# Performance work log

Measured on AMD Instinct MI355X. Metric: run time of the kernel, lower is better.

## Reference

```python
import jax, jax.numpy as jnp
import numpy as np

N = 131072        # total nodes
E = 786432        # total edges (avg degree 6)
NSEG = 128        # number of (graph, config) segments
SEG = N // NSEG   # nodes per segment (equal-size ragged layout)
G = 8             # graphs in batch
S = NSEG // G     # segments (configs) per graph
NF, NCF, OP_DIM = 112, 14, 64
FD = NF + NCF + OP_DIM        # 190 = node_feature_dim
GIN, HID, NOPS = 256, 512, 120


def _linear_init(key, fan_in, fan_out):
    lim = 1.0 / np.sqrt(fan_in)
    return jax.random.uniform(key, (fan_in, fan_out), jnp.float32, -lim, lim)


def setup_inputs() -> dict:
    key = jax.random.key(0)
    ks = jax.random.split(key, 24)
    inp = {
        "node_features": jax.random.normal(ks[0], (N, NF), jnp.float32),
        "node_config_features": jax.random.normal(ks[1], (N, NCF), jnp.float32),
        "node_ops": jax.random.randint(ks[2], (N,), 0, NOPS),
        "edges": jax.random.randint(ks[3], (2, E), 0, N),
        # cumulative exclusive end index of each segment
        "node_separation": (jnp.arange(1, NSEG + 1) * SEG).astype(jnp.int32),
        # which graph each segment belongs to (sorted, S segments per graph)
        "batches": jnp.repeat(jnp.arange(G), S).astype(jnp.int32),
        # parameters
        "emb": jax.random.normal(ks[4], (NOPS, OP_DIM), jnp.float32),
        "W1": _linear_init(ks[5], FD, FD * 2), "b1": jnp.zeros((FD * 2,), jnp.float32),
        "W2": _linear_init(ks[6], FD * 2, GIN), "b2": jnp.zeros((GIN,), jnp.float32),
        "Wl1": _linear_init(ks[7], GIN, HID), "bl1": jnp.zeros((HID,), jnp.float32),
        "Wr1": _linear_init(ks[8], GIN, HID),
        "Wl2": _linear_init(ks[9], HID, HID), "bl2": jnp.zeros((HID,), jnp.float32),
        "Wr2": _linear_init(ks[10], HID, HID),
        "Wl3": _linear_init(ks[11], HID, HID), "bl3": jnp.zeros((HID,), jnp.float32),
        "Wr3": _linear_init(ks[12], HID, HID),
        "Wf": _linear_init(ks[13], HID, 1), "bf": jnp.zeros((1,), jnp.float32),
    }
    return inp


def _l2norm(x, eps=1e-12):
    # F.normalize(p=2): x / max(||x||, eps)
    return x / jnp.maximum(jnp.linalg.norm(x, axis=-1, keepdims=True), eps)


def _sage_conv(x, src, dst, Wl, bl, Wr):
    # mean aggregation of source features onto destination nodes
    msum = jax.ops.segment_sum(x[src], dst, num_segments=N)
    cnt = jax.ops.segment_sum(jnp.ones((src.shape[0],), x.dtype), dst, num_segments=N)
    mean = msum / jnp.maximum(cnt, 1.0)[:, None]
    out = mean @ Wl + bl + x @ Wr   # lin_l(aggr) + lin_r(x), bias only on lin_l
    return _l2norm(out)             # graphsage_normalize=True


def reference(node_features, node_config_features, node_ops, edges, node_separation,
              batches, emb, W1, b1, W2, b2, Wl1, bl1, Wr1, Wl2, bl2, Wr2,
              Wl3, bl3, Wr3, Wf, bf):
    # embedding + feature concat (dropouts are identity at eval)
    op_e = emb[node_ops]                                       # [N, 64]
    x = jnp.concatenate([node_features, node_config_features, op_e], axis=1)  # [N, 190]
    # node feature MLP with L2 normalization over feature dim
    h = jax.nn.relu(x @ W1 + b1)
    h = _l2norm(h @ W2 + b2)                                   # [N, 256]
    # 3-layer GraphSAGE (ReLU between layers, none after last)
    src, dst = edges[0], edges[1]
    h = jax.nn.relu(_sage_conv(h, src, dst, Wl1, bl1, Wr1))
    h = jax.nn.relu(_sage_conv(h, src, dst, Wl2, bl2, Wr2))
    h = _sage_conv(h, src, dst, Wl3, bl3, Wr3)                 # [N, 512]
    # ragged segment-sum: node i belongs to first segment with end index > i
    seg_ids = jnp.searchsorted(node_separation, jnp.arange(N), side="right")
    seg = jax.ops.segment_sum(h, seg_ids, num_segments=NSEG)   # [128, 512]
    # group segments by graph (batches is sorted with S segments per graph)
    within = jnp.arange(NSEG) % S
    agg = jnp.zeros((G, S, HID), h.dtype).at[batches, within].set(seg)
    # final classifier: Linear(512 -> 1), squeeze
    out = (agg @ Wf + bf)[..., 0]                              # [G, S]
    return out
```

## Files before the change

kernel.cpp:

```cpp
#include <hip/hip_runtime.h>
#include <hip/hip_bf16.h>
#include <stdint.h>

#define NN   131072
#define EE   786432
#define NSEGC 128
#define SSC  16
#define NFD  112
#define NCFD 14
#define OPD  64
#define FDIM 190
#define FD2  380
#define GIN  256
#define HID  512

typedef unsigned short u16;
typedef unsigned int   u32;
typedef __attribute__((ext_vector_type(8))) short bf16x8;
typedef __attribute__((ext_vector_type(4))) float f32x4;

__device__ __forceinline__ float b2f(u16 v) { u32 u = ((u32)v) << 16; return __builtin_bit_cast(float, u); }
__device__ __forceinline__ u16 f2b(float f) {
  u32 u = __builtin_bit_cast(u32, f);
  u32 r = (u + 0x7fffu + ((u >> 16) & 1u)) >> 16;
  return (u16)r;
}
__device__ __forceinline__ void unpk8(uint4 q, float* f) {
  f[0] = __builtin_bit_cast(float, q.x << 16);
  f[1] = __builtin_bit_cast(float, q.x & 0xffff0000u);
  f[2] = __builtin_bit_cast(float, q.y << 16);
  f[3] = __builtin_bit_cast(float, q.y & 0xffff0000u);
  f[4] = __builtin_bit_cast(float, q.z << 16);
  f[5] = __builtin_bit_cast(float, q.z & 0xffff0000u);
  f[6] = __builtin_bit_cast(float, q.w << 16);
  f[7] = __builtin_bit_cast(float, q.w & 0xffff0000u);
}
__device__ __forceinline__ void gload16(const void* g, void* lds) {
  __builtin_amdgcn_global_load_lds((const __attribute__((address_space(1))) void*)g,
                                   (__attribute__((address_space(3))) void*)lds, 16, 0, 0);
}

__global__ void k_diag(float* out, float v) { out[threadIdx.x] = v; }

__global__ void k_count(const int* __restrict__ dst, int* __restrict__ deg) {
  int e = blockIdx.x * 256 + threadIdx.x;
  if (e < EE) atomicAdd(&deg[dst[e]], 1);
}

__global__ __launch_bounds__(1024) void k_bsum(const int* __restrict__ deg, int* __restrict__ bsum) {
  __shared__ int ws[16];
  int tid = threadIdx.x;
  int lane = tid & 63, w = tid >> 6;
  int x = deg[blockIdx.x * 1024 + tid];
  #pragma unroll
  for (int off = 32; off; off >>= 1) x += __shfl_xor(x, off, 64);
  if (lane == 0) ws[w] = x;
  __syncthreads();
  if (tid == 0) {
    int t = 0;
    #pragma unroll
    for (int i = 0; i < 16; ++i) t += ws[i];
    bsum[blockIdx.x] = t;
  }
}

__global__ void k_bscan(const int* __restrict__ bsum, int* __restrict__ boff) {
  __shared__ int w0sum;
  int t = threadIdx.x;
  int lane = t & 63;
  int orig = bsum[t];
  int x = orig;
  #pragma unroll
  for (int off = 1; off < 64; off <<= 1) {
    int v = __shfl_up(x, off, 64);
    if (lane >= off) x += v;
  }
  if (t == 63) w0sum = x;
  __syncthreads();
  int excl = x - orig;
  if (t >= 64) excl += w0sum;
  boff[t] = excl;
}

__global__ __launch_bounds__(1024) void k_iptr(const int* __restrict__ deg, const int* __restrict__ boff,
                                               int* __restrict__ indptr) {
  __shared__ int wsum[16];
  int b = blockIdx.x, tid = threadIdx.x;
  int lane = tid & 63, w = tid >> 6;
  int x = deg[b * 1024 + tid];
  #pragma unroll
  for (int off = 1; off < 64; off <<= 1) {
    int v = __shfl_up(x, off, 64);
    if (lane >= off) x += v;
  }
  if (lane == 63) wsum[w] = x;
  __syncthreads();
  int woff = 0;
  #pragma unroll
  for (int i = 0; i < 16; ++i) if (i < w) woff += wsum[i];
  indptr[b * 1024 + tid + 1] = boff[b] + woff + x;
  if (b == 0 && tid == 0) indptr[0] = 0;
}

__global__ void k_fill(const int* __restrict__ src, const int* __restrict__ dst,
                       const int* __restrict__ indptr, int* __restrict__ cur,
                       int* __restrict__ colidx) {
  int e = blockIdx.x * 256 + threadIdx.x;
  if (e < EE) {
    int d = dst[e];
    int p = atomicAdd(&cur[d], 1);
    colidx[indptr[d] + p] = src[e];
  }
}

__global__ void k_wcvt(const float* __restrict__ Wl, const float* __restrict__ Wr,
                       const int kin, u16* __restrict__ WbT) {
  int keff = kin * 2;
  int idx = blockIdx.x * 256 + threadIdx.x;
  int k4 = idx % (keff >> 2);
  int n  = idx / (keff >> 2);
  if (n >= HID) return;
  int k0 = k4 << 2;
  u16 o[4];
  #pragma unroll
  for (int j = 0; j < 4; ++j) {
    int k = k0 + j;
    float v = (k < kin) ? Wl[(size_t)k * HID + n] : Wr[(size_t)(k - kin) * HID + n];
    o[j] = f2b(v);
  }
  uint2 pk;
  pk.x = (u32)o[0] | ((u32)o[1] << 16);
  pk.y = (u32)o[2] | ((u32)o[3] << 16);
  *(uint2*)(WbT + (size_t)n * keff + k0) = pk;
}

__global__ void k_w1cvt(const float* __restrict__ W1, u16* __restrict__ W1p) {
  int t = blockIdx.x / 6, s = blockIdx.x % 6;
  int lane = threadIdx.x;
  int lg = lane >> 4, lc = lane & 15;
  int n = t * 16 + lc;
  bf16x8 v;
  #pragma unroll
  for (int j = 0; j < 8; ++j) {
    int k = s * 32 + lg * 8 + j;
    float f = (k < FDIM && n < FD2) ? W1[(size_t)k * FD2 + n] : 0.f;
    v[j] = (short)f2b(f);
  }
  *(bf16x8*)(W1p + ((size_t)blockIdx.x * 64 + lane) * 8) = v;
}

__global__ void k_w2cvt(const float* __restrict__ W2, u16* __restrict__ W2p) {
  int t = blockIdx.x / 12, s = blockIdx.x % 12;
  int lane = threadIdx.x;
  int lg = lane >> 4, lc = lane & 15;
  int n = t * 16 + lc;
  bf16x8 v;
  #pragma unroll
  for (int j = 0; j < 8; ++j) {
    int k = s * 32 + lg * 8 + j;
    float f = (k < FD2) ? W2[(size_t)k * GIN + n] : 0.f;
    v[j] = (short)f2b(f);
  }
  *(bf16x8*)(W2p + ((size_t)blockIdx.x * 64 + lane) * 8) = v;
}

__global__ __launch_bounds__(512, 4) void k_mlpm(const float* __restrict__ nf, const float* __restrict__ ncf,
                                                 const int* __restrict__ ops, const float* __restrict__ emb,
                                                 const u16* __restrict__ W1p, const float* __restrict__ b1,
                                                 const u16* __restrict__ W2p, const float* __restrict__ b2,
                                                 u16* __restrict__ hA) {
  __shared__ u16 Xs[64 * 200];
  __shared__ u16 H1s[64 * 392];
  const int m0 = blockIdx.x * 64;
  const int tid = threadIdx.x;
  const int lane = tid & 63;
  const int wid = tid >> 6;
  const int lg = lane >> 4;
  const int lc = lane & 15;

  for (int idx = tid; idx < 64 * NFD; idx += 512) {
    int r = idx / NFD, k = idx - r * NFD;
    Xs[r * 200 + k] = f2b(nf[(size_t)(m0 + r) * NFD + k]);
  }
  for (int idx = tid; idx < 64 * NCFD; idx += 512) {
    int r = idx / NCFD, k = idx - r * NCFD;
    Xs[r * 200 + NFD + k] = f2b(ncf[(size_t)(m0 + r) * NCFD + k]);
  }
  for (int idx = tid; idx < 64 * OPD; idx += 512) {
    int r = idx >> 6, k = idx & 63;
    Xs[r * 200 + NFD + NCFD + k] = f2b(emb[(size_t)ops[m0 + r] * OPD + k]);
  }
  if (tid < 128) {
    int r = tid >> 1;
    Xs[r * 200 + FDIM + (tid & 1)] = 0;
  }
  __syncthreads();

  f32x4 acc1[4][3];
  #pragma unroll
  for (int mt = 0; mt < 4; ++mt)
    #pragma unroll
    for (int nt = 0; nt < 3; ++nt) acc1[mt][nt] = (f32x4){0.f, 0.f, 0.f, 0.f};
  #pragma unroll
  for (int s = 0; s < 6; ++s) {
    bf16x8 af[4];
    #pragma unroll
    for (int mt = 0; mt < 4; ++mt)
      af[mt] = *(const bf16x8*)(Xs + (mt * 16 + lc) * 200 + s * 32 + lg * 8);
    #pragma unroll
    for (int nt = 0; nt < 3; ++nt) {
      int t = wid * 3 + nt;
      bf16x8 bfr = *(const bf16x8*)(W1p + ((size_t)(t * 6 + s) * 64 + lane) * 8);
      #pragma unroll
      for (int mt = 0; mt < 4; ++mt)
        acc1[mt][nt] = __builtin_amdgcn_mfma_f32_16x16x32_bf16(af[mt], bfr, acc1[mt][nt], 0, 0, 0);
    }
  }
  #pragma unroll
  for (int nt = 0; nt < 3; ++nt) {
    int n = (wid * 3 + nt) * 16 + lc;
    float bias = b1[n < FD2 ? n : FD2 - 1];
    #pragma unroll
    for (int mt = 0; mt < 4; ++mt)
      #pragma unroll
      for (int r = 0; r < 4; ++r) {
        float v = acc1[mt][nt][r] + bias;
        H1s[(mt * 16 + lg * 4 + r) * 392 + n] = f2b(v > 0.f ? v : 0.f);
      }
  }
  __syncthreads();

  f32x4 acc2[4][2];
  #pragma unroll
  for (int mt = 0; mt < 4; ++mt)
    #pragma unroll
    for (int nt = 0; nt < 2; ++nt) acc2[mt][nt] = (f32x4){0.f, 0.f, 0.f, 0.f};
  #pragma unroll
  for (int s = 0; s < 12; ++s) {
    bf16x8 af[4];
    #pragma unroll
    for (int mt = 0; mt < 4; ++mt)
      af[mt] = *(const bf16x8*)(H1s + (mt * 16 + lc) * 392 + s * 32 + lg * 8);
    #pragma unroll
    for (int nt = 0; nt < 2; ++nt) {
      int t = wid * 2 + nt;
      bf16x8 bfr = *(const bf16x8*)(W2p + ((size_t)(t * 12 + s) * 64 + lane) * 8);
      #pragma unroll
      for (int mt = 0; mt < 4; ++mt)
        acc2[mt][nt] = __builtin_amdgcn_mfma_f32_16x16x32_bf16(af[mt], bfr, acc2[mt][nt], 0, 0, 0);
    }
  }
  float* ssq = (float*)Xs;
  float bias2[2];
  #pragma unroll
  for (int nt = 0; nt < 2; ++nt) bias2[nt] = b2[(wid * 2 + nt) * 16 + lc];
  #pragma unroll
  for (int mt = 0; mt < 4; ++mt)
    #pragma unroll
    for (int r = 0; r < 4; ++r) {
      float s = 0.f;
      #pragma unroll
      for (int nt = 0; nt < 2; ++nt) {
        float v = acc2[mt][nt][r] + bias2[nt];
        acc2[mt][nt][r] = v;
        s += v * v;
      }
      s += __shfl_xor(s, 1, 64);
      s += __shfl_xor(s, 2, 64);
      s += __shfl_xor(s, 4, 64);
      s += __shfl_xor(s, 8, 64);
      if (lc == 0) ssq[(mt * 16 + lg * 4 + r) * 8 + wid] = s;
    }
  __syncthreads();
  float scl[4][4];
  #pragma unroll
  for (int mt = 0; mt < 4; ++mt)
    #pragma unroll
    for (int r = 0; r < 4; ++r) {
      const float* p = ssq + (mt * 16 + lg * 4 + r) * 8;
      float t = ((p[0] + p[1]) + (p[2] + p[3])) + ((p[4] + p[5]) + (p[6] + p[7]));
      scl[mt][r] = 1.f / fmaxf(sqrtf(t), 1e-12f);
    }
  u16* T = H1s;
  #pragma unroll
  for (int mt = 0; mt < 4; ++mt)
    #pragma unroll
    for (int nt = 0; nt < 2; ++nt)
      #pragma unroll
      for (int r = 0; r < 4; ++r)
        T[(mt * 16 + lg * 4 + r) * 264 + (wid * 2 + nt) * 16 + lc] =
            f2b(acc2[mt][nt][r] * scl[mt][r]);
  __syncthreads();
  #pragma unroll
  for (int it = 0; it < 4; ++it) {
    int flat = it * 512 + tid;
    int row = flat >> 5, ch = flat & 31;
    uint4 v = *(const uint4*)(T + row * 264 + ch * 8);
    *(uint4*)(hA + (size_t)(m0 + row) * HID + ch * 8) = v;
  }
}

template<int F>
__global__ __launch_bounds__(256) void k_agg(const u16* __restrict__ h, int8_t* __restrict__ M8,
                                             float* __restrict__ Msc,
                                             const int* __restrict__ indptr, const int* __restrict__ colidx) {
  int d = blockIdx.x * 4 + (threadIdx.x >> 6);
  int lane = threadIdx.x & 63;
  float acc[F];
  #pragma unroll
  for (int i = 0; i < F; ++i) acc[i] = 0.f;
  int s0 = indptr[d], s1 = indptr[d + 1];
  int e = s0;
  for (; e + 3 < s1; e += 4) {
    int sa = colidx[e], sb = colidx[e + 1], sc = colidx[e + 2], sd = colidx[e + 3];
    if constexpr (F == 8) {
      uint4 qa = *(const uint4*)(h + (size_t)sa * HID + lane * 8);
      uint4 qb = *(const uint4*)(h + (size_t)sb * HID + lane * 8);
      uint4 qc = *(const uint4*)(h + (size_t)sc * HID + lane * 8);
      uint4 qd = *(const uint4*)(h + (size_t)sd * HID + lane * 8);
      float fa[8], fb[8], fc[8], fd[8];
      unpk8(qa, fa); unpk8(qb, fb); unpk8(qc, fc); unpk8(qd, fd);
      #pragma unroll
      for (int i = 0; i < 8; ++i) acc[i] += (fa[i] + fb[i]) + (fc[i] + fd[i]);
    } else {
      uint2 qa = *(const uint2*)(h + (size_t)sa * HID + lane * 4);
      uint2 qb = *(const uint2*)(h + (size_t)sb * HID + lane * 4);
      uint2 qc = *(const uint2*)(h + (size_t)sc * HID + lane * 4);
      uint2 qd = *(const uint2*)(h + (size_t)sd * HID + lane * 4);
      acc[0] += (__builtin_bit_cast(float, qa.x << 16) + __builtin_bit_cast(float, qb.x << 16))
              + (__builtin_bit_cast(float, qc.x << 16) + __builtin_bit_cast(float, qd.x << 16));
      acc[1] += (__builtin_bit_cast(float, qa.x & 0xffff0000u) + __builtin_bit_cast(float, qb.x & 0xffff0000u))
              + (__builtin_bit_cast(float, qc.x & 0xffff0000u) + __builtin_bit_cast(float, qd.x & 0xffff0000u));
      acc[2] += (__builtin_bit_cast(float, qa.y << 16) + __builtin_bit_cast(float, qb.y << 16))
              + (__builtin_bit_cast(float, qc.y << 16) + __builtin_bit_cast(float, qd.y << 16));
      acc[3] += (__builtin_bit_cast(float, qa.y & 0xffff0000u) + __builtin_bit_cast(float, qb.y & 0xffff0000u))
              + (__builtin_bit_cast(float, qc.y & 0xffff0000u) + __builtin_bit_cast(float, qd.y & 0xffff0000u));
    }
  }
  for (; e < s1; ++e) {
    int s = colidx[e];
    const u16* p = h + (size_t)s * HID + lane * F;
    if constexpr (F == 8) {
      uint4 q = *(const uint4*)p;
      float f[8]; unpk8(q, f);
      #pragma unroll
      for (int i = 0; i < 8; ++i) acc[i] += f[i];
    } else {
      uint2 q = *(const uint2*)p;
      acc[0] += __builtin_bit_cast(float, q.x << 16);
      acc[1] += __builtin_bit_cast(float, q.x & 0xffff0000u);
      acc[2] += __builtin_bit_cast(float, q.y << 16);
      acc[3] += __builtin_bit_cast(float, q.y & 0xffff0000u);
    }
  }
  int dgi = s1 - s0;
  float inv = 1.f / (float)(dgi > 1 ? dgi : 1);
  float m = 0.f;
  #pragma unroll
  for (int i = 0; i < F; ++i) { acc[i] *= inv; m = fmaxf(m, fabsf(acc[i])); }
  #pragma unroll
  for (int off = 32; off; off >>= 1) m = fmaxf(m, __shfl_xor(m, off, 64));
  float scale = (m > 0.f) ? (m / 127.f) : 1.f;
  float rscl = 1.f / scale;
  int q[F];
  #pragma unroll
  for (int i = 0; i < F; ++i) {
    int t = (int)__builtin_rintf(acc[i] * rscl);
    q[i] = t < -127 ? -127 : (t > 127 ? 127 : t);
  }
  int8_t* row = M8 + (size_t)d * HID;
  if constexpr (F == 8) {
    uint2 o;
    o.x = (u32)(q[0] & 255) | ((u32)(q[1] & 255) << 8) | ((u32)(q[2] & 255) << 16) | ((u32)(q[3] & 255) << 24);
    o.y = (u32)(q[4] & 255) | ((u32)(q[5] & 255) << 8) | ((u32)(q[6] & 255) << 16) | ((u32)(q[7] & 255) << 24);
    *(uint2*)(row + lane * 8) = o;
  } else {
    u32 o = (u32)(q[0] & 255) | ((u32)(q[1] & 255) << 8) | ((u32)(q[2] & 255) << 16) | ((u32)(q[3] & 255) << 24);
    *(u32*)(row + lane * 4) = o;
  }
  if (lane == 0) Msc[d] = scale;
}

template<int KIN, bool RELU, bool FUSE>
__global__ __launch_bounds__(512, 4) void k_sagem(const u16* __restrict__ hA,
                                                  const int8_t* __restrict__ M8,
                                                  const float* __restrict__ Msc,
                                                  const u16* __restrict__ WbT,
                                                  const float* __restrict__ bl,
                                                  u16* __restrict__ outp,
                                                  const float* __restrict__ Wf,
                                                  float* __restrict__ partial) {
  constexpr int KEFF = 2 * KIN;
  constexpr int KSTEPS = KEFF / 64;
  __shared__ unsigned char smem[73728];
  u16* As = (u16*)smem;
  u16* Bs = (u16*)(smem + 8192);
  const int m0 = blockIdx.x * 64;
  const int tid = threadIdx.x;
  const int lane = tid & 63;
  const int wid = tid >> 6;
  const int lg = lane >> 4;
  const int lc = lane & 15;

  f32x4 acc[4][4];
  #pragma unroll
  for (int mt = 0; mt < 4; ++mt)
    #pragma unroll
    for (int nt = 0; nt < 4; ++nt) acc[mt][nt] = (f32x4){0.f, 0.f, 0.f, 0.f};

  for (int t = 0; t < KSTEPS; ++t) {
    const int kt = t * 64;
    __syncthreads();
    if (kt < KIN) {
      int r = tid >> 3, c = tid & 7;
      int row = m0 + r;
      float sc = Msc[row];
      uint2 q = *(const uint2*)(M8 + (size_t)row * HID + kt + c * 8);
      float f[8];
      #pragma unroll
      for (int i = 0; i < 4; ++i) f[i]     = (float)((int)(q.x << (24 - 8 * i)) >> 24) * sc;
      #pragma unroll
      for (int i = 0; i < 4; ++i) f[4 + i] = (float)((int)(q.y << (24 - 8 * i)) >> 24) * sc;
      bf16x8 v;
      #pragma unroll
      for (int i = 0; i < 8; ++i) v[i] = (short)f2b(f[i]);
      *(bf16x8*)(As + r * 64 + ((c ^ (r & 7)) << 3)) = v;
    } else {
      int r = wid * 8 + (lane >> 3);
      int c = (lane & 7) ^ (lane >> 3);
      gload16(hA + (size_t)(m0 + r) * HID + (kt - KIN) + c * 8, As + wid * 512);
    }
    #pragma unroll
    for (int i = 0; i < 8; ++i) {
      int R = wid * 64 + i * 8;
      int n = R + (lane >> 3);
      int c = (lane & 7) ^ (lane >> 3);
      gload16(WbT + (size_t)n * KEFF + kt + c * 8, Bs + R * 64);
    }
    __syncthreads();
    __builtin_amdgcn_s_setprio(1);
    #pragma unroll
    for (int s = 0; s < 2; ++s) {
      bf16x8 af[4];
      #pragma unroll
      for (int mt = 0; mt < 4; ++mt) {
        int r = mt * 16 + lc;
        int c = (s * 4 + lg) ^ (r & 7);
        af[mt] = *(const bf16x8*)(As + r * 64 + (c << 3));
      }
      #pragma unroll
      for (int nt = 0; nt < 4; ++nt) {
        int n = wid * 64 + nt * 16 + lc;
        int c = (s * 4 + lg) ^ (n & 7);
        bf16x8 bfr = *(const bf16x8*)(Bs + n * 64 + (c << 3));
        #pragma unroll
        for (int mt = 0; mt < 4; ++mt)
          acc[mt][nt] = __builtin_amdgcn_mfma_f32_16x16x32_bf16(af[mt], bfr, acc[mt][nt], 0, 0, 0);
      }
    }
    __builtin_amdgcn_s_setprio(0);
  }
  __syncthreads();

  float* ssq = (float*)(smem + 66560);
  float bias[4];
  #pragma unroll
  for (int nt = 0; nt < 4; ++nt) bias[nt] = bl[wid * 64 + nt * 16 + lc];
  #pragma unroll
  for (int mt = 0; mt < 4; ++mt) {
    #pragma unroll
    for (int r = 0; r < 4; ++r) {
      float s = 0.f;
      #pragma unroll
      for (int nt = 0; nt < 4; ++nt) {
        float v = acc[mt][nt][r] + bias[nt];
        acc[mt][nt][r] = v;
        s += v * v;
      }
      s += __shfl_xor(s, 1, 64);
      s += __shfl_xor(s, 2, 64);
      s += __shfl_xor(s, 4, 64);
      s += __shfl_xor(s, 8, 64);
      if (lc == 0) ssq[(mt * 16 + lg * 4 + r) * 8 + wid] = s;
    }
  }
  __syncthreads();
  float scl[4][4];
  #pragma unroll
  for (int mt = 0; mt < 4; ++mt)
    #pragma unroll
    for (int r = 0; r < 4; ++r) {
      const float* p = ssq + (mt * 16 + lg * 4 + r) * 8;
      float t = ((p[0] + p[1]) + (p[2] + p[3])) + ((p[4] + p[5]) + (p[6] + p[7]));
      scl[mt][r] = 1.f / fmaxf(sqrtf(t), 1e-12f);
    }
  if constexpr (FUSE) {
    float wf[4];
    #pragma unroll
    for (int nt = 0; nt < 4; ++nt) wf[nt] = Wf[wid * 64 + nt * 16 + lc];
    float s = 0.f;
    #pragma unroll
    for (int mt = 0; mt < 4; ++mt)
      #pragma unroll
      for (int r = 0; r < 4; ++r) {
        float rs = scl[mt][r];
        #pragma unroll
        for (int nt = 0; nt < 4; ++nt) s += acc[mt][nt][r] * rs * wf[nt];
      }
    #pragma unroll
    for (int off = 32; off; off >>= 1) s += __shfl_xor(s, off, 64);
    float* red = (float*)(smem + 68608);
    if (lane == 0) red[wid] = s;
    __syncthreads();
    if (tid == 0) {
      float t = 0.f;
      #pragma unroll
      for (int i = 0; i < 8; ++i) t += red[i];
      partial[blockIdx.x] = t;
    }
  } else {
    u16* T = (u16*)smem;
    #pragma unroll
    for (int mt = 0; mt < 4; ++mt)
      #pragma unroll
      for (int r = 0; r < 4; ++r) {
        int trow = mt * 16 + lg * 4 + r;
        #pragma unroll
        for (int nt = 0; nt < 4; ++nt) {
          float v = acc[mt][nt][r] * scl[mt][r];
          if (RELU) v = v > 0.f ? v : 0.f;
          T[trow * 520 + wid * 64 + nt * 16 + lc] = f2b(v);
        }
      }
    __syncthreads();
    #pragma unroll
    for (int it = 0; it < 8; ++it) {
      int flat = it * 512 + tid;
      int row = flat >> 6, ch = flat & 63;
      uint4 v = *(const uint4*)(T + row * 520 + ch * 8);
      *(uint4*)(outp + (size_t)(m0 + row) * HID + ch * 8) = v;
    }
  }
}

__global__ void k_fred(const float* __restrict__ partial, const float* __restrict__ bfp,
                       const int* __restrict__ batches, float* __restrict__ outp) {
  int s = threadIdx.x;
  float t = bfp[0];
  #pragma unroll
  for (int i = 0; i < 16; ++i) t += partial[s * 16 + i];
  outp[batches[s] * SSC + (s & (SSC - 1))] = t;
}

extern "C" void kernel_launch(void* const* d_in, const int* in_sizes, int n_in,
                              void* d_out, int out_size, void* d_ws, size_t ws_size,
                              hipStream_t stream) {
  const float* nf   = (const float*)d_in[0];
  const float* ncf  = (const float*)d_in[1];
  const int*   ops  = (const int*)d_in[2];
  const int*   edges = (const int*)d_in[3];
  const int*   sep  = (const int*)d_in[4];
  const int*   batches = (const int*)d_in[5];
  const float* emb  = (const float*)d_in[6];
  const float* W1   = (const float*)d_in[7];  const float* b1 = (const float*)d_in[8];
  const float* W2   = (const float*)d_in[9];  const float* b2 = (const float*)d_in[10];
  const float* Wl1  = (const float*)d_in[11]; const float* bl1 = (const float*)d_in[12]; const float* Wr1 = (const float*)d_in[13];
  const float* Wl2  = (const float*)d_in[14]; const float* bl2 = (const float*)d_in[15]; const float* Wr2 = (const float*)d_in[16];
  const float* Wl3  = (const float*)d_in[17]; const float* bl3 = (const float*)d_in[18]; const float* Wr3 = (const float*)d_in[19];
  const float* Wf   = (const float*)d_in[20]; const float* bfp = (const float*)d_in[21];
  float* outp = (float*)d_out;

  const size_t OFF_M8  = (size_t)NN * HID * 2;
  const size_t OFF_MSC = OFF_M8 + (size_t)NN * HID;
  const size_t OFF_IP  = OFF_MSC + (size_t)NN * 4;
  const size_t OFF_CI  = OFF_IP + (((size_t)(NN + 1) * 4 + 255) & ~(size_t)255);
  const size_t OFF_W1  = OFF_CI + (size_t)EE * 4;
  const size_t OFF_W2  = OFF_W1 + (size_t)HID * 512 * 2;
  const size_t OFF_W3  = OFF_W2 + (size_t)HID * 1024 * 2;
  const size_t NEED    = OFF_W3 + (size_t)HID * 1024 * 2;
  if (ws_size < NEED) {
    k_diag<<<1, 128, 0, stream>>>(outp, (float)((double)ws_size / 1048576.0));
    return;
  }

  char* ws = (char*)d_ws;
  u16*    hA     = (u16*)ws;
  int8_t* M8     = (int8_t*)(ws + OFF_M8);
  float*  Msc    = (float*)(ws + OFF_MSC);
  int*    indptr = (int*)(ws + OFF_IP);
  int*    colidx = (int*)(ws + OFF_CI);
  u16*    Wb1    = (u16*)(ws + OFF_W1);
  u16*    Wb2    = (u16*)(ws + OFF_W2);
  u16*    Wb3    = (u16*)(ws + OFF_W3);
  int*    deg    = (int*)hA;
  int*    cur    = (int*)(ws + (size_t)NN * 4);
  int*    bsum   = (int*)(ws + (size_t)NN * 8);
  int*    boff   = (int*)(ws + (size_t)NN * 8 + 512);
  u16*    W1p    = (u16*)M8;
  u16*    W2p    = (u16*)(ws + OFF_M8 + 262144);
  float*  partials = (float*)Wb1;

  const int* esrc = edges;
  const int* edst = edges + EE;

  hipMemsetAsync(deg, 0, (size_t)NN * 4, stream);
  k_count<<<EE / 256, 256, 0, stream>>>(edst, deg);
  k_bsum<<<NN / 1024, 1024, 0, stream>>>(deg, bsum);
  k_bscan<<<1, 128, 0, stream>>>(bsum, boff);
  k_iptr<<<NN / 1024, 1024, 0, stream>>>(deg, boff, indptr);
  hipMemsetAsync(cur, 0, (size_t)NN * 4, stream);
  k_fill<<<EE / 256, 256, 0, stream>>>(esrc, edst, indptr, cur, colidx);

  k_wcvt<<<256, 256, 0, stream>>>(Wl1, Wr1, GIN, Wb1);
  k_wcvt<<<512, 256, 0, stream>>>(Wl2, Wr2, HID, Wb2);
  k_wcvt<<<512, 256, 0, stream>>>(Wl3, Wr3, HID, Wb3);
  k_w1cvt<<<144, 64, 0, stream>>>(W1, W1p);
  k_w2cvt<<<192, 64, 0, stream>>>(W2, W2p);

  k_mlpm<<<NN / 64, 512, 0, stream>>>(nf, ncf, ops, emb, W1p, b1, W2p, b2, hA);

  k_agg<4><<<NN / 4, 256, 0, stream>>>(hA, M8, Msc, indptr, colidx);
  k_sagem<GIN, true, false><<<NN / 64, 512, 0, stream>>>(hA, M8, Msc, Wb1, bl1, hA, nullptr, nullptr);
  k_agg<8><<<NN / 4, 256, 0, stream>>>(hA, M8, Msc, indptr, colidx);
  k_sagem<HID, true, false><<<NN / 64, 512, 0, stream>>>(hA, M8, Msc, Wb2, bl2, hA, nullptr, nullptr);
  k_agg<8><<<NN / 4, 256, 0, stream>>>(hA, M8, Msc, indptr, colidx);
  k_sagem<HID, false, true><<<NN / 64, 512, 0, stream>>>(hA, M8, Msc, Wb3, bl3, hA, Wf, partials);

  k_fred<<<1, 128, 0, stream>>>(partials, bfp, batches, outp);
}
```

Baseline: 955.9 us.

## Store node features as int8 and aggregated means as bf16

Node features written by the MLP and SAGE kernels are now quantized to int8 with a per-row scale. The gather-aggregation kernel reads these int8 rows, which shrinks the random-gather traffic over edges by half, and writes the mean as bf16 instead of requantizing it. The GEMM kernel swaps which operand is loaded asynchronously (bf16 mean) and which is dequantized (int8 self features). This trades gather bandwidth for extra quantization error on the self and neighbor features, plus some dequantize ALU work.

```diff
diff --git a/kernel.cpp b/kernel.cpp
--- a/kernel.cpp
+++ b/kernel.cpp
@@ -25,15 +25,19 @@
   u32 r = (u + 0x7fffu + ((u >> 16) & 1u)) >> 16;
   return (u16)r;
 }
-__device__ __forceinline__ void unpk8(uint4 q, float* f) {
-  f[0] = __builtin_bit_cast(float, q.x << 16);
-  f[1] = __builtin_bit_cast(float, q.x & 0xffff0000u);
-  f[2] = __builtin_bit_cast(float, q.y << 16);
-  f[3] = __builtin_bit_cast(float, q.y & 0xffff0000u);
-  f[4] = __builtin_bit_cast(float, q.z << 16);
-  f[5] = __builtin_bit_cast(float, q.z & 0xffff0000u);
-  f[6] = __builtin_bit_cast(float, q.w << 16);
-  f[7] = __builtin_bit_cast(float, q.w & 0xffff0000u);
+__device__ __forceinline__ void dq8(uint2 q, float sc, float* f) {
+  #pragma unroll
+  for (int i = 0; i < 4; ++i) f[i]     = (float)((int)(q.x << (24 - 8 * i)) >> 24) * sc;
+  #pragma unroll
+  for (int i = 0; i < 4; ++i) f[4 + i] = (float)((int)(q.y << (24 - 8 * i)) >> 24) * sc;
+}
+__device__ __forceinline__ void dq4(u32 q, float sc, float* f) {
+  #pragma unroll
+  for (int i = 0; i < 4; ++i) f[i] = (float)((int)(q << (24 - 8 * i)) >> 24) * sc;
+}
+__device__ __forceinline__ int q8(float v, float qinv) {
+  int t = (int)__builtin_rintf(v * qinv);
+  return t < -127 ? -127 : (t > 127 ? 127 : t);
 }
 __device__ __forceinline__ void gload16(const void* g, void* lds) {
   __builtin_amdgcn_global_load_lds((const __attribute__((address_space(1))) void*)g,
@@ -168,7 +172,7 @@
                                                  const int* __restrict__ ops, const float* __restrict__ emb,
                                                  const u16* __restrict__ W1p, const float* __restrict__ b1,
                                                  const u16* __restrict__ W2p, const float* __restrict__ b2,
-                                                 u16* __restrict__ hA) {
+                                                 int8_t* __restrict__ h8, float* __restrict__ hsc) {
   __shared__ u16 Xs[64 * 200];
   __shared__ u16 H1s[64 * 392];
   const int m0 = blockIdx.x * 64;
@@ -250,7 +254,9 @@
         acc2[mt][nt] = __builtin_amdgcn_mfma_f32_16x16x32_bf16(af[mt], bfr, acc2[mt][nt], 0, 0, 0);
     }
   }
-  float* ssq = (float*)Xs;
+  float* ssq  = (float*)Xs;
+  float* tmx  = (float*)Xs + 512;
+  float* qsc  = (float*)Xs + 1024;
   float bias2[2];
   #pragma unroll
   for (int nt = 0; nt < 2; ++nt) bias2[nt] = b2[(wid * 2 + nt) * 16 + lc];
@@ -258,18 +264,23 @@
   for (int mt = 0; mt < 4; ++mt)
     #pragma unroll
     for (int r = 0; r < 4; ++r) {
-      float s = 0.f;
+      float s = 0.f, mx = 0.f;
       #pragma unroll
       for (int nt = 0; nt < 2; ++nt) {
         float v = acc2[mt][nt][r] + bias2[nt];
         acc2[mt][nt][r] = v;
         s += v * v;
-      }
-      s += __shfl_xor(s, 1, 64);
-      s += __shfl_xor(s, 2, 64);
-      s += __shfl_xor(s, 4, 64);
-      s += __shfl_xor(s, 8, 64);
-      if (lc == 0) ssq[(mt * 16 + lg * 4 + r) * 8 + wid] = s;
+        mx = fmaxf(mx, fabsf(v));
+      }
+      #pragma unroll
+      for (int off = 1; off < 16; off <<= 1) {
+        s += __shfl_xor(s, off, 64);
+        mx = fmaxf(mx, __shfl_xor(mx, off, 64));
+      }
+      if (lc == 0) {
+        ssq[(mt * 16 + lg * 4 + r) * 8 + wid] = s;
+        tmx[(mt * 16 + lg * 4 + r) * 8 + wid] = mx;
+      }
     }
   __syncthreads();
   float scl[4][4];
@@ -277,9 +288,19 @@
   for (int mt = 0; mt < 4; ++mt)
     #pragma unroll
     for (int r = 0; r < 4; ++r) {
-      const float* p = ssq + (mt * 16 + lg * 4 + r) * 8;
+      int row = mt * 16 + lg * 4 + r;
+      const float* p = ssq + row * 8;
+      const float* q = tmx + row * 8;
       float t = ((p[0] + p[1]) + (p[2] + p[3])) + ((p[4] + p[5]) + (p[6] + p[7]));
-      scl[mt][r] = 1.f / fmaxf(sqrtf(t), 1e-12f);
+      float m = fmaxf(fmaxf(fmaxf(q[0], q[1]), fmaxf(q[2], q[3])),
+                      fmaxf(fmaxf(q[4], q[5]), fmaxf(q[6], q[7])));
+      float sc = 1.f / fmaxf(sqrtf(t), 1e-12f);
+      scl[mt][r] = sc;
+      if (wid == 0 && lc == 0) {
+        float qs = m * sc / 127.f;
+        qsc[row] = (qs > 0.f) ? 1.f / qs : 0.f;
+        hsc[m0 + row] = qs;
+      }
     }
   u16* T = H1s;
   #pragma unroll
@@ -295,14 +316,23 @@
   for (int it = 0; it < 4; ++it) {
     int flat = it * 512 + tid;
     int row = flat >> 5, ch = flat & 31;
+    float qi = qsc[row];
     uint4 v = *(const uint4*)(T + row * 264 + ch * 8);
-    *(uint4*)(hA + (size_t)(m0 + row) * HID + ch * 8) = v;
+    int qv[8];
+    qv[0] = q8(b2f((u16)v.x), qi);        qv[1] = q8(b2f((u16)(v.x >> 16)), qi);
+    qv[2] = q8(b2f((u16)v.y), qi);        qv[3] = q8(b2f((u16)(v.y >> 16)), qi);
+    qv[4] = q8(b2f((u16)v.z), qi);        qv[5] = q8(b2f((u16)(v.z >> 16)), qi);
+    qv[6] = q8(b2f((u16)v.w), qi);        qv[7] = q8(b2f((u16)(v.w >> 16)), qi);
+    uint2 o;
+    o.x = (u32)(qv[0] & 255) | ((u32)(qv[1] & 255) << 8) | ((u32)(qv[2] & 255) << 16) | ((u32)(qv[3] & 255) << 24);
+    o.y = (u32)(qv[4] & 255) | ((u32)(qv[5] & 255) << 8) | ((u32)(qv[6] & 255) << 16) | ((u32)(qv[7] & 255) << 24);
+    *(uint2*)(h8 + (size_t)(m0 + row) * HID + ch * 8) = o;
   }
 }
 
 template<int F>
-__global__ __launch_bounds__(256) void k_agg(const u16* __restrict__ h, int8_t* __restrict__ M8,
-                                             float* __restrict__ Msc,
+__global__ __launch_bounds__(256) void k_agg(const int8_t* __restrict__ h8, const float* __restrict__ hsc,
+                                             u16* __restrict__ Mb,
                                              const int* __restrict__ indptr, const int* __restrict__ colidx) {
   int d = blockIdx.x * 4 + (threadIdx.x >> 6);
   int lane = threadIdx.x & 63;
@@ -313,81 +343,60 @@
   int e = s0;
   for (; e + 3 < s1; e += 4) {
     int sa = colidx[e], sb = colidx[e + 1], sc = colidx[e + 2], sd = colidx[e + 3];
+    float fa[F], fb[F], fc[F], fd[F];
     if constexpr (F == 8) {
-      uint4 qa = *(const uint4*)(h + (size_t)sa * HID + lane * 8);
-      uint4 qb = *(const uint4*)(h + (size_t)sb * HID + lane * 8);
-      uint4 qc = *(const uint4*)(h + (size_t)sc * HID + lane * 8);
-      uint4 qd = *(const uint4*)(h + (size_t)sd * HID + lane * 8);
-      float fa[8], fb[8], fc[8], fd[8];
-      unpk8(qa, fa); unpk8(qb, fb); unpk8(qc, fc); unpk8(qd, fd);
-      #pragma unroll
-      for (int i = 0; i < 8; ++i) acc[i] += (fa[i] + fb[i]) + (fc[i] + fd[i]);
+      uint2 qa = *(const uint2*)(h8 + (size_t)sa * HID + lane * 8);
+      uint2 qb = *(const uint2*)(h8 + (size_t)sb * HID + lane * 8);
+      uint2 qc = *(const uint2*)(h8 + (size_t)sc * HID + lane * 8);
+      uint2 qd = *(const uint2*)(h8 + (size_t)sd * HID + lane * 8);
+      dq8(qa, hsc[sa], fa); dq8(qb, hsc[sb], fb); dq8(qc, hsc[sc], fc); dq8(qd, hsc[sd], fd);
     } else {
-      uint2 qa = *(const uint2*)(h + (size_t)sa * HID + lane * 4);
-      uint2 qb = *(const uint2*)(h + (size_t)sb * HID + lane * 4);
-      uint2 qc = *(const uint2*)(h + (size_t)sc * HID + lane * 4);
-      uint2 qd = *(const uint2*)(h + (size_t)sd * HID + lane * 4);
-      acc[0] += (__builtin_bit_cast(float, qa.x << 16) + __builtin_bit_cast(float, qb.x << 16))
-              + (__builtin_bit_cast(float, qc.x << 16) + __builtin_bit_cast(float, qd.x << 16));
-      acc[1] += (__builtin_bit_cast(float, qa.x & 0xffff0000u) + __builtin_bit_cast(float, qb.x & 0xffff0000u))
-              + (__builtin_bit_cast(float, qc.x & 0xffff0000u) + __builtin_bit_cast(float, qd.x & 0xffff0000u));
-      acc[2] += (__builtin_bit_cast(float, qa.y << 16) + __builtin_bit_cast(float, qb.y << 16))
-              + (__builtin_bit_cast(float, qc.y << 16) + __builtin_bit_cast(float, qd.y << 16));
-      acc[3] += (__builtin_bit_cast(float, qa.y & 0xffff0000u) + __builtin_bit_cast(float, qb.y & 0xffff0000u))
-              + (__builtin_bit_cast(float, qc.y & 0xffff0000u) + __builtin_bit_cast(float, qd.y & 0xffff0000u));
-    }
+      u32 qa = *(const u32*)(h8 + (size_t)sa * HID + lane * 4);
+      u32 qb = *(const u32*)(h8 + (size_t)sb * HID + lane * 4);
+      u32 qc = *(const u32*)(h8 + (size_t)sc * HID + lane * 4);
+      u32 qd = *(const u32*)(h8 + (size_t)sd * HID + lane * 4);
+      dq4(qa, hsc[sa], fa); dq4(qb, hsc[sb], fb); dq4(qc, hsc[sc], fc); dq4(qd, hsc[sd], fd);
+    }
+    #pragma unroll
+    for (int i = 0; i < F; ++i) acc[i] += (fa[i] + fb[i]) + (fc[i] + fd[i]);
   }
   for (; e < s1; ++e) {
     int s = colidx[e];
-    const u16* p = h + (size_t)s * HID + lane * F;
+    float f[F];
     if constexpr (F == 8) {
-      uint4 q = *(const uint4*)p;
-      float f[8]; unpk8(q, f);
-      #pragma unroll
-      for (int i = 0; i < 8; ++i) acc[i] += f[i];
+      uint2 q = *(const uint2*)(h8 + (size_t)s * HID + lane * 8);
+      dq8(q, hsc[s], f);
     } else {
-      uint2 q = *(const uint2*)p;
-      acc[0] += __builtin_bit_cast(float, q.x << 16);
-      acc[1] += __builtin_bit_cast(float, q.x & 0xffff0000u);
-      acc[2] += __builtin_bit_cast(float, q.y << 16);
-      acc[3] += __builtin_bit_cast(float, q.y & 0xffff0000u);
-    }
+      u32 q = *(const u32*)(h8 + (size_t)s * HID + lane * 4);
+      dq4(q, hsc[s], f);
+    }
+    #pragma unroll
+    for (int i = 0; i < F; ++i) acc[i] += f[i];
   }
   int dgi = s1 - s0;
   float inv = 1.f / (float)(dgi > 1 ? dgi : 1);
-  float m = 0.f;
-  #pragma unroll
-  for (int i = 0; i < F; ++i) { acc[i] *= inv; m = fmaxf(m, fabsf(acc[i])); }
-  #pragma unroll
-  for (int off = 32; off; off >>= 1) m = fmaxf(m, __shfl_xor(m, off, 64));
-  float scale = (m > 0.f) ? (m / 127.f) : 1.f;
-  float rscl = 1.f / scale;
-  int q[F];
-  #pragma unroll
-  for (int i = 0; i < F; ++i) {
-    int t = (int)__builtin_rintf(acc[i] * rscl);
-    q[i] = t < -127 ? -127 : (t > 127 ? 127 : t);
-  }
-  int8_t* row = M8 + (size_t)d * HID;
+  u16* row = Mb + (size_t)d * HID;
   if constexpr (F == 8) {
+    uint4 o;
+    o.x = (u32)f2b(acc[0] * inv) | ((u32)f2b(acc[1] * inv) << 16);
+    o.y = (u32)f2b(acc[2] * inv) | ((u32)f2b(acc[3] * inv) << 16);
+    o.z = (u32)f2b(acc[4] * inv) | ((u32)f2b(acc[5] * inv) << 16);
+    o.w = (u32)f2b(acc[6] * inv) | ((u32)f2b(acc[7] * inv) << 16);
+    *(uint4*)(row + lane * 8) = o;
+  } else {
     uint2 o;
-    o.x = (u32)(q[0] & 255) | ((u32)(q[1] & 255) << 8) | ((u32)(q[2] & 255) << 16) | ((u32)(q[3] & 255) << 24);
-    o.y = (u32)(q[4] & 255) | ((u32)(q[5] & 255) << 8) | ((u32)(q[6] & 255) << 16) | ((u32)(q[7] & 255) << 24);
-    *(uint2*)(row + lane * 8) = o;
-  } else {
-    u32 o = (u32)(q[0] & 255) | ((u32)(q[1] & 255) << 8) | ((u32)(q[2] & 255) << 16) | ((u32)(q[3] & 255) << 24);
-    *(u32*)(row + lane * 4) = o;
-  }
-  if (lane == 0) Msc[d] = scale;
+    o.x = (u32)f2b(acc[0] * inv) | ((u32)f2b(acc[1] * inv) << 16);
+    o.y = (u32)f2b(acc[2] * inv) | ((u32)f2b(acc[3] * inv) << 16);
+    *(uint2*)(row + lane * 4) = o;
+  }
 }
 
 template<int KIN, bool RELU, bool FUSE>
-__global__ __launch_bounds__(512, 4) void k_sagem(const u16* __restrict__ hA,
-                                                  const int8_t* __restrict__ M8,
-                                                  const float* __restrict__ Msc,
+__global__ __launch_bounds__(512, 4) void k_sagem(int8_t* __restrict__ h8,
+                                                  float* __restrict__ hsc,
+                                                  const u16* __restrict__ Mb,
                                                   const u16* __restrict__ WbT,
                                                   const float* __restrict__ bl,
-                                                  u16* __restrict__ outp,
                                                   const float* __restrict__ Wf,
                                                   float* __restrict__ partial) {
   constexpr int KEFF = 2 * KIN;
@@ -412,23 +421,20 @@
     const int kt = t * 64;
     __syncthreads();
     if (kt < KIN) {
+      int r = wid * 8 + (lane >> 3);
+      int c = (lane & 7) ^ (lane >> 3);
+      gload16(Mb + (size_t)(m0 + r) * HID + kt + c * 8, As + wid * 512);
+    } else {
       int r = tid >> 3, c = tid & 7;
       int row = m0 + r;
-      float sc = Msc[row];
-      uint2 q = *(const uint2*)(M8 + (size_t)row * HID + kt + c * 8);
+      float sc = hsc[row];
+      uint2 q = *(const uint2*)(h8 + (size_t)row * HID + (kt - KIN) + c * 8);
       float f[8];
-      #pragma unroll
-      for (int i = 0; i < 4; ++i) f[i]     = (float)((int)(q.x << (24 - 8 * i)) >> 24) * sc;
-      #pragma unroll
-      for (int i = 0; i < 4; ++i) f[4 + i] = (float)((int)(q.y << (24 - 8 * i)) >> 24) * sc;
+      dq8(q, sc, f);
       bf16x8 v;
       #pragma unroll
       for (int i = 0; i < 8; ++i) v[i] = (short)f2b(f[i]);
       *(bf16x8*)(As + r * 64 + ((c ^ (r & 7)) << 3)) = v;
-    } else {
-      int r = wid * 8 + (lane >> 3);
-      int c = (lane & 7) ^ (lane >> 3);
-      gload16(hA + (size_t)(m0 + r) * HID + (kt - KIN) + c * 8, As + wid * 512);
     }
     #pragma unroll
     for (int i = 0; i < 8; ++i) {
@@ -463,6 +469,8 @@
   __syncthreads();
 
   float* ssq = (float*)(smem + 66560);
+  float* tmx = (float*)(smem + 68608);
+  float* qsc = (float*)(smem + 70656);
   float bias[4];
   #pragma unroll
   for (int nt = 0; nt < 4; ++nt) bias[nt] = bl[wid * 64 + nt * 16 + lc];
@@ -470,18 +478,23 @@
   for (int mt = 0; mt < 4; ++mt) {
     #pragma unroll
     for (int r = 0; r < 4; ++r) {
-      float s = 0.f;
+      float s = 0.f, mx = 0.f;
       #pragma unroll
       for (int nt = 0; nt < 4; ++nt) {
         float v = acc[mt][nt][r] + bias[nt];
         acc[mt][nt][r] = v;
         s += v * v;
-      }
-      s += __shfl_xor(s, 1, 64);
-      s += __shfl_xor(s, 2, 64);
-      s += __shfl_xor(s, 4, 64);
-      s += __shfl_xor(s, 8, 64);
-      if (lc == 0) ssq[(mt * 16 + lg * 4 + r) * 8 + wid] = s;
+        mx = fmaxf(mx, fabsf(v));
+      }
+      #pragma unroll
+      for (int off = 1; off < 16; off <<= 1) {
+        s += __shfl_xor(s, off, 64);
+        if (!FUSE) mx = fmaxf(mx, __shfl_xor(mx, off, 64));
+      }
+      if (lc == 0) {
+        ssq[(mt * 16 + lg * 4 + r) * 8 + wid] = s;
+        if (!FUSE) tmx[(mt * 16 + lg * 4 + r) * 8 + wid] = mx;
+      }
     }
   }
   __syncthreads();
@@ -490,9 +503,21 @@
   for (int mt = 0; mt < 4; ++mt)
     #pragma unroll
     for (int r = 0; r < 4; ++r) {
-      const float* p = ssq + (mt * 16 + lg * 4 + r) * 8;
+      int row = mt * 16 + lg * 4 + r;
+      const float* p = ssq + row * 8;
       float t = ((p[0] + p[1]) + (p[2] + p[3])) + ((p[4] + p[5]) + (p[6] + p[7]));
-      scl[mt][r] = 1.f / fmaxf(sqrtf(t), 1e-12f);
+      float sc = 1.f / fmaxf(sqrtf(t), 1e-12f);
+      scl[mt][r] = sc;
+      if (!FUSE) {
+        const float* q = tmx + row * 8;
+        float m = fmaxf(fmaxf(fmaxf(q[0], q[1]), fmaxf(q[2], q[3])),
+                        fmaxf(fmaxf(q[4], q[5]), fmaxf(q[6], q[7])));
+        if (wid == 0 && lc == 0) {
+          float qs = m * sc / 127.f;
+          qsc[row] = (qs > 0.f) ? 1.f / qs : 0.f;
+          hsc[m0 + row] = qs;
+        }
+      }
     }
   if constexpr (FUSE) {
     float wf[4];
@@ -537,8 +562,17 @@
     for (int it = 0; it < 8; ++it) {
       int flat = it * 512 + tid;
       int row = flat >> 6, ch = flat & 63;
+      float qi = qsc[row];
       uint4 v = *(const uint4*)(T + row * 520 + ch * 8);
-      *(uint4*)(outp + (size_t)(m0 + row) * HID + ch * 8) = v;
+      int qv[8];
+      qv[0] = q8(b2f((u16)v.x), qi);        qv[1] = q8(b2f((u16)(v.x >> 16)), qi);
+      qv[2] = q8(b2f((u16)v.y), qi);        qv[3] = q8(b2f((u16)(v.y >> 16)), qi);
+      qv[4] = q8(b2f((u16)v.z), qi);        qv[5] = q8(b2f((u16)(v.z >> 16)), qi);
+      qv[6] = q8(b2f((u16)v.w), qi);        qv[7] = q8(b2f((u16)(v.w >> 16)), qi);
+      uint2 o;
+      o.x = (u32)(qv[0] & 255) | ((u32)(qv[1] & 255) << 8) | ((u32)(qv[2] & 255) << 16) | ((u32)(qv[3] & 255) << 24);
+      o.y = (u32)(qv[4] & 255) | ((u32)(qv[5] & 255) << 8) | ((u32)(qv[6] & 255) << 16) | ((u32)(qv[7] & 255) << 24);
+      *(uint2*)(h8 + (size_t)(m0 + row) * HID + ch * 8) = o;
     }
   }
 }
@@ -570,9 +604,9 @@
   const float* Wf   = (const float*)d_in[20]; const float* bfp = (const float*)d_in[21];
   float* outp = (float*)d_out;
 
-  const size_t OFF_M8  = (size_t)NN * HID * 2;
-  const size_t OFF_MSC = OFF_M8 + (size_t)NN * HID;
-  const size_t OFF_IP  = OFF_MSC + (size_t)NN * 4;
+  const size_t OFF_MB  = (size_t)NN * HID;
+  const size_t OFF_HSC = OFF_MB + (size_t)NN * HID * 2;
+  const size_t OFF_IP  = OFF_HSC + (size_t)NN * 4;
   const size_t OFF_CI  = OFF_IP + (((size_t)(NN + 1) * 4 + 255) & ~(size_t)255);
   const size_t OFF_W1  = OFF_CI + (size_t)EE * 4;
   const size_t OFF_W2  = OFF_W1 + (size_t)HID * 512 * 2;
@@ -584,20 +618,20 @@
   }
 
   char* ws = (char*)d_ws;
-  u16*    hA     = (u16*)ws;
-  int8_t* M8     = (int8_t*)(ws + OFF_M8);
-  float*  Msc    = (float*)(ws + OFF_MSC);
+  int8_t* h8     = (int8_t*)ws;
+  u16*    Mb     = (u16*)(ws + OFF_MB);
+  float*  hsc    = (float*)(ws + OFF_HSC);
   int*    indptr = (int*)(ws + OFF_IP);
   int*    colidx = (int*)(ws + OFF_CI);
   u16*    Wb1    = (u16*)(ws + OFF_W1);
   u16*    Wb2    = (u16*)(ws + OFF_W2);
   u16*    Wb3    = (u16*)(ws + OFF_W3);
-  int*    deg    = (int*)hA;
+  int*    deg    = (int*)h8;
   int*    cur    = (int*)(ws + (size_t)NN * 4);
   int*    bsum   = (int*)(ws + (size_t)NN * 8);
   int*    boff   = (int*)(ws + (size_t)NN * 8 + 512);
-  u16*    W1p    = (u16*)M8;
-  u16*    W2p    = (u16*)(ws + OFF_M8 + 262144);
+  u16*    W1p    = (u16*)Mb;
+  u16*    W2p    = (u16*)(ws + OFF_MB + 262144);
   float*  partials = (float*)Wb1;
 
   const int* esrc = edges;
@@ -617,14 +651,14 @@
   k_w1cvt<<<144, 64, 0, stream>>>(W1, W1p);
   k_w2cvt<<<192, 64, 0, stream>>>(W2, W2p);
 
-  k_mlpm<<<NN / 64, 512, 0, stream>>>(nf, ncf, ops, emb, W1p, b1, W2p, b2, hA);
-
-  k_agg<4><<<NN / 4, 256, 0, stream>>>(hA, M8, Msc, indptr, colidx);
-  k_sagem<GIN, true, false><<<NN / 64, 512, 0, stream>>>(hA, M8, Msc, Wb1, bl1, hA, nullptr, nullptr);
-  k_agg<8><<<NN / 4, 256, 0, stream>>>(hA, M8, Msc, indptr, colidx);
-  k_sagem<HID, true, false><<<NN / 64, 512, 0, stream>>>(hA, M8, Msc, Wb2, bl2, hA, nullptr, nullptr);
-  k_agg<8><<<NN / 4, 256, 0, stream>>>(hA, M8, Msc, indptr, colidx);
-  k_sagem<HID, false, true><<<NN / 64, 512, 0, stream>>>(hA, M8, Msc, Wb3, bl3, hA, Wf, partials);
+  k_mlpm<<<NN / 64, 512, 0, stream>>>(nf, ncf, ops, emb, W1p, b1, W2p, b2, h8, hsc);
+
+  k_agg<4><<<NN / 4, 256, 0, stream>>>(h8, hsc, Mb, indptr, colidx);
+  k_sagem<GIN, true, false><<<NN / 64, 512, 0, stream>>>(h8, hsc, Mb, Wb1, bl1, nullptr, nullptr);
+  k_agg<8><<<NN / 4, 256, 0, stream>>>(h8, hsc, Mb, indptr, colidx);
+  k_sagem<HID, true, false><<<NN / 64, 512, 0, stream>>>(h8, hsc, Mb, Wb2, bl2, nullptr, nullptr);
+  k_agg<8><<<NN / 4, 256, 0, stream>>>(h8, hsc, Mb, indptr, colidx);
+  k_sagem<HID, false, true><<<NN / 64, 512, 0, stream>>>(h8, hsc, Mb, Wb3, bl3, Wf, partials);
 
   k_fred<<<1, 128, 0, stream>>>(partials, bfp, batches, outp);
 }
```

Measured after the change: 932.6 us. 2.4% less time.
